# Performance work log

Measured on AMD Instinct MI355X. Metric: run time of the kernel, lower is better.

Reference implementation:

```python
import jax, jax.numpy as jnp
import numpy as np

EMBED = 1024
HEADS = 16
HEAD_DIM = EMBED // HEADS


def setup_inputs() -> dict:
    key = jax.random.key(0)
    ks = jax.random.split(key, 8)
    N, S = 4, 2048
    values = jax.random.normal(ks[0], (N, S, EMBED), dtype=jnp.float32)
    queries = jax.random.normal(ks[1], (N, S, EMBED), dtype=jnp.float32)
    keys = jax.random.normal(ks[2], (N, S, EMBED), dtype=jnp.float32)
    mask = jax.random.randint(ks[3], (N, 1, S, S), 0, 2, dtype=jnp.int32)
    sc = 1.0 / np.sqrt(HEAD_DIM)
    Wv = jax.random.normal(ks[4], (HEAD_DIM, HEAD_DIM), dtype=jnp.float32) * sc
    Wk = jax.random.normal(ks[5], (HEAD_DIM, HEAD_DIM), dtype=jnp.float32) * sc
    Wq = jax.random.normal(ks[6], (HEAD_DIM, HEAD_DIM), dtype=jnp.float32) * sc
    Wo = jax.random.normal(ks[7], (EMBED, EMBED), dtype=jnp.float32) * (1.0 / np.sqrt(EMBED))
    bo = jnp.zeros((EMBED,), dtype=jnp.float32)
    return {"values": values, "queries": queries, "keys": keys, "mask": mask,
            "Wv": Wv, "Wk": Wk, "Wq": Wq, "Wo": Wo, "bo": bo}


def reference(values, queries, keys, mask, Wv, Wk, Wq, Wo, bo):
    N, S, _ = queries.shape
    # split heads: (N, len, H, D)
    v = values.reshape(N, -1, HEADS, HEAD_DIM)
    k = keys.reshape(N, -1, HEADS, HEAD_DIM)
    q = queries.reshape(N, -1, HEADS, HEAD_DIM)
    # per-head linear projections (nn.Linear: y = x @ W.T, no bias)
    v = jnp.einsum('nlhd,ed->nlhe', v, Wv)
    k = jnp.einsum('nlhd,ed->nlhe', k, Wk)
    q = jnp.einsum('nlhd,ed->nlhe', q, Wq)
    # energy: (N, H, q_len, k_len)
    energy = jnp.einsum('nqhd,nkhd->nhqk', q, k)
    energy = jnp.where(mask == 0, jnp.float32(-1e20), energy)
    # non-standard scale: sqrt(embed_size), applied after masking
    attn = jax.nn.softmax(energy / jnp.sqrt(jnp.float32(EMBED)), axis=3)
    out = jnp.einsum('nhql,nlhd->nqhd', attn, v).reshape(N, S, EMBED)
    return out @ Wo.T + bo
```

## Files before the change

### kernel.cpp

```cpp
#include <hip/hip_runtime.h>
#include <hip/hip_bf16.h>

#define NBATCH 4
#define SEQ    2048
#define EMBED  1024
#define HEADS  16
#define HD     64

typedef __attribute__((ext_vector_type(8))) short bf16x8;
typedef __attribute__((ext_vector_type(4))) float f32x4;

__device__ __forceinline__ short f2bf(float f) {
  union { float f; unsigned u; } v; v.f = f;
  unsigned r = v.u + 0x7fffu + ((v.u >> 16) & 1u);
  return (short)(r >> 16);
}

__device__ __forceinline__ unsigned pkbf(float a, float b) {
#if __has_builtin(__builtin_amdgcn_cvt_pk_bf16_f32)
  typedef __attribute__((ext_vector_type(2))) __bf16 bf16x2_t;
  bf16x2_t r = __builtin_amdgcn_cvt_pk_bf16_f32(a, b);
  union { bf16x2_t v; unsigned u; } cv; cv.v = r; return cv.u;
#else
  return (unsigned)(unsigned short)f2bf(a) | ((unsigned)(unsigned short)f2bf(b) << 16);
#endif
}

typedef __attribute__((address_space(1))) const void gas_void;
typedef __attribute__((address_space(3))) void las_void;
__device__ __forceinline__ void glds16(const void* g, void* l) {
  __builtin_amdgcn_global_load_lds((gas_void*)g, (las_void*)l, 16, 0, 0);
}

#define C2 0.04508422f

__global__ __launch_bounds__(256) void cvt_all(
    const float* __restrict__ Wo, const float* __restrict__ Wq,
    const float* __restrict__ Wk, const float* __restrict__ Wv,
    short* __restrict__ dWo, short* __restrict__ dWq,
    short* __restrict__ dWk, short* __restrict__ dWv)
{
  int e = (blockIdx.x * 256 + threadIdx.x) * 4;
  const float* src; short* dst; int off; float sc = 1.0f;
  if (e < EMBED * EMBED) { src = Wo; dst = dWo; off = e; }
  else {
    int j = e - EMBED * EMBED;
    if      (j < 4096)  { src = Wq; dst = dWq; off = j; sc = C2; }
    else if (j < 8192)  { src = Wk; dst = dWk; off = j - 4096; }
    else if (j < 12288) { src = Wv; dst = dWv; off = j - 8192; }
    else return;
  }
  float4 v = *(const float4*)(src + off);
  ushort4 p;
  p.x = (unsigned short)f2bf(v.x * sc);
  p.y = (unsigned short)f2bf(v.y * sc);
  p.z = (unsigned short)f2bf(v.z * sc);
  p.w = (unsigned short)f2bf(v.w * sc);
  *(ushort4*)(dst + off) = p;
}

__global__ __launch_bounds__(256) void mask_pack(const int* __restrict__ mask,
                                                 unsigned long long* __restrict__ bits) {
  long long t = (long long)blockIdx.x * 256 + threadIdx.x;
  int lane = threadIdx.x & 63;
  int m = mask[t];
  unsigned long long b = __ballot(m != 0);
  if (lane == 0) bits[t >> 6] = b;
}

__global__ __launch_bounds__(256) void proj_kernel(
    const float* __restrict__ srcQ, const float* __restrict__ srcK, const float* __restrict__ srcV,
    const short* __restrict__ WbQ, const short* __restrict__ WbK, const short* __restrict__ WbV,
    short* __restrict__ Qp, short* __restrict__ Kp, short* __restrict__ Vt)
{
  int rt = blockIdx.x;
  int h  = blockIdx.y;
  int mz = blockIdx.z;
  const float* src = (mz == 0) ? srcQ : ((mz == 1) ? srcK : srcV);
  const short* Wb  = (mz == 0) ? WbQ : ((mz == 1) ? WbK : WbV);

  __shared__ __align__(16) short At[64][72];

  int tid = threadIdx.x;
  int r0 = rt * 64;
  for (int idx = tid; idx < 64 * 16; idx += 256) {
    int row = idx >> 4;
    int c4  = idx & 15;
    float4 v = *(const float4*)(src + (long long)(r0 + row) * EMBED + h * HD + c4 * 4);
    uint2 pk2;
    pk2.x = pkbf(v.x, v.y);
    pk2.y = pkbf(v.z, v.w);
    *(uint2*)&At[row][c4 * 4] = pk2;
  }
  __syncthreads();

  int lane = tid & 63, w = tid >> 6, quad = lane >> 4, l15 = lane & 15;

  bf16x8 af0 = *(const bf16x8*)&At[w * 16 + l15][quad * 8];
  bf16x8 af1 = *(const bf16x8*)&At[w * 16 + l15][32 + quad * 8];

  f32x4 acc[4];
  for (int cg = 0; cg < 4; cg++) {
    acc[cg] = (f32x4){0.f, 0.f, 0.f, 0.f};
    bf16x8 b0 = *(const bf16x8*)(Wb + (cg * 16 + l15) * 64 + quad * 8);
    bf16x8 b1 = *(const bf16x8*)(Wb + (cg * 16 + l15) * 64 + 32 + quad * 8);
    acc[cg] = __builtin_amdgcn_mfma_f32_16x16x32_bf16(af0, b0, acc[cg], 0, 0, 0);
    acc[cg] = __builtin_amdgcn_mfma_f32_16x16x32_bf16(af1, b1, acc[cg], 0, 0, 0);
  }

  int rloc = w * 16 + quad * 4;
  if (mz < 2) {
    short* dst = (mz == 0) ? Qp : Kp;
    for (int cg = 0; cg < 4; cg++) {
      for (int reg = 0; reg < 4; reg++) {
        int r = r0 + rloc + reg;
        int n = r >> 11, s = r & 2047;
        dst[((long long)(n * HEADS + h) * SEQ + s) * HD + cg * 16 + l15] = f2bf(acc[cg][reg]);
      }
    }
  } else {
    int r = r0 + rloc;
    int n = r >> 11, s = r & 2047;
    for (int cg = 0; cg < 4; cg++) {
      int d = cg * 16 + l15;
      uint2 pk2;
      pk2.x = pkbf(acc[cg][0], acc[cg][1]);
      pk2.y = pkbf(acc[cg][2], acc[cg][3]);
      *(uint2*)(Vt + ((long long)(n * HEADS + h) * HD + d) * SEQ + s) = pk2;
    }
  }
}

__global__ __launch_bounds__(512) void attn_kernel(
    const short* __restrict__ Qp, const short* __restrict__ Kp, const short* __restrict__ Vt,
    const unsigned long long* __restrict__ mbits, short* __restrict__ AO)
{
  int qt = blockIdx.x, h = blockIdx.y, nb = blockIdx.z;
  int q0 = qt * 128;

  __shared__ __align__(16) short KtL[64 * 64];
  __shared__ __align__(16) short VsL[64 * 64];
  __shared__ __align__(16) short Pls[8][16][72];

  int tid = threadIdx.x, lane = tid & 63, w = tid >> 6, quad = lane >> 4, l15 = lane & 15;
  int g8 = lane & 7, r8 = lane >> 3;
  int swz = g8 ^ r8;
  int s3 = l15 & 7;
  int o0 = (quad ^ s3) * 16;
  int o1 = ((quad + 4) ^ s3) * 16;

  long long nh = (long long)(nb * HEADS + h);
  const char* Kb = (const char*)(Kp + nh * SEQ * HD);
  const char* Vb = (const char*)(Vt + nh * HD * SEQ);
  const short* Qbase = Qp + (nh * SEQ + q0) * HD;

  int qrow = q0 + w * 16 + l15;

  int kgo = (w * 8 + r8) * 128 + swz * 16;
  int vgo = (w * 8 + r8) * 4096 + swz * 16;
  unsigned klo = (unsigned)(w * 8) * 128;

  const unsigned long long* mptr = mbits + ((long long)nb * SEQ + qrow) * 32;

  bf16x8 qf0 = *(const bf16x8*)(Qbase + (w * 16 + l15) * HD + quad * 8);
  bf16x8 qf1 = *(const bf16x8*)(Qbase + (w * 16 + l15) * HD + 32 + quad * 8);

  f32x4 O[4];
#pragma unroll
  for (int i = 0; i < 4; i++) O[i] = (f32x4){0.f, 0.f, 0.f, 0.f};
  float lsum = 0.f;

  for (int kt = 0; kt < 32; kt++) {
    int k0 = kt * 64;
    __syncthreads();
    glds16(Kb + k0 * 128 + kgo, (char*)KtL + klo);
    glds16(Vb + k0 * 2   + vgo, (char*)VsL + klo);
    unsigned long long mrow = mptr[kt];
    __syncthreads();

    const char* KB = (const char*)KtL;
    f32x4 sA[4];
#pragma unroll
    for (int cg = 0; cg < 4; cg++) {
      bf16x8 kf0 = *(const bf16x8*)(KB + (cg * 16 + l15) * 128 + o0);
      bf16x8 kf1 = *(const bf16x8*)(KB + (cg * 16 + l15) * 128 + o1);
      f32x4 a = (f32x4){0.f, 0.f, 0.f, 0.f};
      a = __builtin_amdgcn_mfma_f32_16x16x32_bf16(kf0, qf0, a, 0, 0, 0);
      a = __builtin_amdgcn_mfma_f32_16x16x32_bf16(kf1, qf1, a, 0, 0, 0);
      sA[cg] = a;
    }

    unsigned mlo = (unsigned)mrow, mhi = (unsigned)(mrow >> 32);
    unsigned sh = (unsigned)(quad * 4);
    unsigned nibs[4];
    nibs[0] = (mlo >> sh) & 0xFu;
    nibs[1] = (mlo >> (sh + 16)) & 0xFu;
    nibs[2] = (mhi >> sh) & 0xFu;
    nibs[3] = (mhi >> (sh + 16)) & 0xFu;

    float ssum = 0.f;
#pragma unroll
    for (int cg = 0; cg < 4; cg++) {
#pragma unroll
      for (int r = 0; r < 4; r++) {
        float p = __builtin_amdgcn_exp2f(sA[cg][r]);
        p = (nibs[cg] & (1u << r)) ? p : 0.f;
        sA[cg][r] = p;
        ssum += p;
      }
    }
    lsum += ssum;

#pragma unroll
    for (int cg = 0; cg < 4; cg++) {
      uint2 pk;
      pk.x = pkbf(sA[cg][0], sA[cg][1]);
      pk.y = pkbf(sA[cg][2], sA[cg][3]);
      *(uint2*)&Pls[w][l15][cg * 16 + quad * 4] = pk;
    }

    bf16x8 pa0 = *(const bf16x8*)&Pls[w][l15][quad * 8];
    bf16x8 pa1 = *(const bf16x8*)&Pls[w][l15][32 + quad * 8];

    const char* VB = (const char*)VsL;
#pragma unroll
    for (int cg = 0; cg < 4; cg++) {
      bf16x8 vf0 = *(const bf16x8*)(VB + (cg * 16 + l15) * 128 + o0);
      bf16x8 vf1 = *(const bf16x8*)(VB + (cg * 16 + l15) * 128 + o1);
      O[cg] = __builtin_amdgcn_mfma_f32_16x16x32_bf16(vf0, pa0, O[cg], 0, 0, 0);
      O[cg] = __builtin_amdgcn_mfma_f32_16x16x32_bf16(vf1, pa1, O[cg], 0, 0, 0);
    }
  }

  lsum += __shfl_xor(lsum, 16);
  lsum += __shfl_xor(lsum, 32);
  float inv = 1.f / lsum;
  short* aoRow = AO + ((long long)nb * SEQ + qrow) * EMBED + h * HD;
#pragma unroll
  for (int cg = 0; cg < 4; cg++) {
    uint2 pk;
    pk.x = pkbf(O[cg][0] * inv, O[cg][1] * inv);
    pk.y = pkbf(O[cg][2] * inv, O[cg][3] * inv);
    *(uint2*)(aoRow + cg * 16 + quad * 4) = pk;
  }
}

__global__ __launch_bounds__(256) void outproj_kernel(
    const short* __restrict__ AO, const short* __restrict__ Wob,
    const float* __restrict__ bo, float* __restrict__ out)
{
  int rt = blockIdx.x, ct = blockIdx.y;
  __shared__ __align__(16) short AtL[128 * 64];
  __shared__ __align__(16) short BtL[128 * 64];

  int tid = threadIdx.x, lane = tid & 63, w = tid >> 6, quad = lane >> 4, l15 = lane & 15;
  int g8 = lane & 7, r8 = lane >> 3;
  int swz = g8 ^ r8;
  int s3 = l15 & 7;
  int o0 = (quad ^ s3) * 16;
  int o1 = ((quad + 4) ^ s3) * 16;

  int r0 = rt * 128, c0 = ct * 128;
  int wr = (w >> 1) * 64, wc = (w & 1) * 64;

  const char* Abase = (const char*)AO  + (long long)(r0 + w * 8 + r8) * 2048 + swz * 16;
  const char* Bbase = (const char*)Wob + (long long)(c0 + w * 8 + r8) * 2048 + swz * 16;
  unsigned lbase = (unsigned)(w * 8) * 128;

  f32x4 acc[4][4];
#pragma unroll
  for (int mi = 0; mi < 4; mi++)
#pragma unroll
    for (int ni = 0; ni < 4; ni++) acc[mi][ni] = (f32x4){0.f, 0.f, 0.f, 0.f};

  for (int kc = 0; kc < 16; kc++) {
    __syncthreads();
#pragma unroll
    for (int i = 0; i < 4; i++) {
      glds16(Abase + (long long)i * 32 * 2048 + kc * 128, (char*)AtL + lbase + i * 32 * 128);
      glds16(Bbase + (long long)i * 32 * 2048 + kc * 128, (char*)BtL + lbase + i * 32 * 128);
    }
    __syncthreads();

    const char* AB = (const char*)AtL;
    const char* BB = (const char*)BtL;
    bf16x8 af[4][2], bf[4][2];
#pragma unroll
    for (int mi = 0; mi < 4; mi++) {
      int r = wr + mi * 16 + l15;
      af[mi][0] = *(const bf16x8*)(AB + r * 128 + o0);
      af[mi][1] = *(const bf16x8*)(AB + r * 128 + o1);
    }
#pragma unroll
    for (int ni = 0; ni < 4; ni++) {
      int r = wc + ni * 16 + l15;
      bf[ni][0] = *(const bf16x8*)(BB + r * 128 + o0);
      bf[ni][1] = *(const bf16x8*)(BB + r * 128 + o1);
    }
#pragma unroll
    for (int mi = 0; mi < 4; mi++)
#pragma unroll
      for (int ni = 0; ni < 4; ni++) {
        acc[mi][ni] = __builtin_amdgcn_mfma_f32_16x16x32_bf16(af[mi][0], bf[ni][0], acc[mi][ni], 0, 0, 0);
        acc[mi][ni] = __builtin_amdgcn_mfma_f32_16x16x32_bf16(af[mi][1], bf[ni][1], acc[mi][ni], 0, 0, 0);
      }
  }

#pragma unroll
  for (int ni = 0; ni < 4; ni++) {
    float b = bo[c0 + wc + ni * 16 + l15];
#pragma unroll
    for (int mi = 0; mi < 4; mi++)
#pragma unroll
      for (int reg = 0; reg < 4; reg++) {
        int r = r0 + wr + mi * 16 + quad * 4 + reg;
        out[(long long)r * EMBED + c0 + wc + ni * 16 + l15] = acc[mi][ni][reg] + b;
      }
  }
}

extern "C" void kernel_launch(void* const* d_in, const int* in_sizes, int n_in,
                              void* d_out, int out_size, void* d_ws, size_t ws_size,
                              hipStream_t stream) {
  const float* values  = (const float*)d_in[0];
  const float* queries = (const float*)d_in[1];
  const float* keys    = (const float*)d_in[2];
  const int*   mask    = (const int*)d_in[3];
  const float* Wv = (const float*)d_in[4];
  const float* Wk = (const float*)d_in[5];
  const float* Wq = (const float*)d_in[6];
  const float* Wo = (const float*)d_in[7];
  const float* bo = (const float*)d_in[8];
  float* out = (float*)d_out;

  char* ws = (char*)d_ws;
  size_t off = 0;
  const size_t PROJ_BYTES = (size_t)NBATCH * HEADS * SEQ * HD * 2;
  short* Qp = (short*)(ws + off); off += PROJ_BYTES;
  short* Kp = (short*)(ws + off); off += PROJ_BYTES;
  short* Vt = (short*)(ws + off); off += PROJ_BYTES;
  short* AO = (short*)(ws + off); off += PROJ_BYTES;
  unsigned long long* mbits = (unsigned long long*)(ws + off);
  off += (size_t)NBATCH * SEQ * (SEQ / 64) * 8;
  short* Wob = (short*)(ws + off); off += (size_t)EMBED * EMBED * 2;
  short* WbQ = (short*)(ws + off); off += HD * HD * 2;
  short* WbK = (short*)(ws + off); off += HD * HD * 2;
  short* WbV = (short*)(ws + off); off += HD * HD * 2;

  cvt_all<<<dim3((EMBED * EMBED + 3 * HD * HD) / 4 / 256), dim3(256), 0, stream>>>(
      Wo, Wq, Wk, Wv, Wob, WbQ, WbK, WbV);

  mask_pack<<<dim3((NBATCH * SEQ * SEQ) / 256), dim3(256), 0, stream>>>(mask, mbits);

  proj_kernel<<<dim3((NBATCH * SEQ) / 64, HEADS, 3), dim3(256), 0, stream>>>(
      queries, keys, values, WbQ, WbK, WbV, Qp, Kp, Vt);

  attn_kernel<<<dim3(SEQ / 128, HEADS, NBATCH), dim3(512), 0, stream>>>(Qp, Kp, Vt, mbits, AO);

  outproj_kernel<<<dim3((NBATCH * SEQ) / 128, EMBED / 128), dim3(256), 0, stream>>>(AO, Wob, bo, out);
}
```

Baseline: 378.3 us.

## Double-buffer K/V tiles in LDS and prefetch next tile during compute

K and V LDS tiles become two-slot buffers. The next tile's global-to-LDS copy and its mask word are issued right after a single barrier, so they overlap with the current tile's QK, softmax and PV work. This drops the second per-iteration barrier. The per-row probability sum is also restructured as a tree instead of a serial chain. The cost is double the K/V LDS footprint, which may reduce occupancy, and correctness now relies on the barrier's implicit wait on outstanding loads.

```diff
diff --git a/kernel.cpp b/kernel.cpp
--- a/kernel.cpp
+++ b/kernel.cpp
@@ -138,8 +138,8 @@
   int qt = blockIdx.x, h = blockIdx.y, nb = blockIdx.z;
   int q0 = qt * 128;
 
-  __shared__ __align__(16) short KtL[64 * 64];
-  __shared__ __align__(16) short VsL[64 * 64];
+  __shared__ __align__(16) short KtL[2][64 * 64];
+  __shared__ __align__(16) short VsL[2][64 * 64];
   __shared__ __align__(16) short Pls[8][16][72];
 
   int tid = threadIdx.x, lane = tid & 63, w = tid >> 6, quad = lane >> 4, l15 = lane & 15;
@@ -170,15 +170,22 @@
   for (int i = 0; i < 4; i++) O[i] = (f32x4){0.f, 0.f, 0.f, 0.f};
   float lsum = 0.f;
 
+  glds16(Kb + kgo, (char*)KtL[0] + klo);
+  glds16(Vb + vgo, (char*)VsL[0] + klo);
+  unsigned long long mrow_nxt = mptr[0];
+
   for (int kt = 0; kt < 32; kt++) {
-    int k0 = kt * 64;
     __syncthreads();
-    glds16(Kb + k0 * 128 + kgo, (char*)KtL + klo);
-    glds16(Vb + k0 * 2   + vgo, (char*)VsL + klo);
-    unsigned long long mrow = mptr[kt];
-    __syncthreads();
-
-    const char* KB = (const char*)KtL;
+
+    if (kt < 31) {
+      int k1 = (kt + 1) * 64;
+      glds16(Kb + k1 * 128 + kgo, (char*)KtL[(kt + 1) & 1] + klo);
+      glds16(Vb + k1 * 2   + vgo, (char*)VsL[(kt + 1) & 1] + klo);
+    }
+    unsigned long long mrow = mrow_nxt;
+    if (kt < 31) mrow_nxt = mptr[kt + 1];
+
+    const char* KB = (const char*)KtL[kt & 1];
     f32x4 sA[4];
 #pragma unroll
     for (int cg = 0; cg < 4; cg++) {
@@ -198,7 +205,6 @@
     nibs[2] = (mhi >> sh) & 0xFu;
     nibs[3] = (mhi >> (sh + 16)) & 0xFu;
 
-    float ssum = 0.f;
 #pragma unroll
     for (int cg = 0; cg < 4; cg++) {
 #pragma unroll
@@ -206,10 +212,15 @@
         float p = __builtin_amdgcn_exp2f(sA[cg][r]);
         p = (nibs[cg] & (1u << r)) ? p : 0.f;
         sA[cg][r] = p;
-        ssum += p;
       }
     }
-    lsum += ssum;
+    {
+      float a0 = (sA[0][0] + sA[0][1]) + (sA[0][2] + sA[0][3]);
+      float a1 = (sA[1][0] + sA[1][1]) + (sA[1][2] + sA[1][3]);
+      float a2 = (sA[2][0] + sA[2][1]) + (sA[2][2] + sA[2][3]);
+      float a3 = (sA[3][0] + sA[3][1]) + (sA[3][2] + sA[3][3]);
+      lsum += (a0 + a1) + (a2 + a3);
+    }
 
 #pragma unroll
     for (int cg = 0; cg < 4; cg++) {
@@ -222,7 +233,7 @@
     bf16x8 pa0 = *(const bf16x8*)&Pls[w][l15][quad * 8];
     bf16x8 pa1 = *(const bf16x8*)&Pls[w][l15][32 + quad * 8];
 
-    const char* VB = (const char*)VsL;
+    const char* VB = (const char*)VsL[kt & 1];
 #pragma unroll
     for (int cg = 0; cg < 4; cg++) {
       bf16x8 vf0 = *(const bf16x8*)(VB + (cg * 16 + l15) * 128 + o0);
```

New measurement: 377.4 us. About the same (-0.2%).
